# Kernel tuning notes

Measured on AMD Instinct MI355X. Metric: run time of the kernel, lower is better.

## Reference

```python
import jax, jax.numpy as jnp
import numpy as np

B, N, D, S = 16, 128, 128, 128   # batch, n_nodes, node/edge feat dim, state_dim
MP_INT = 256
UP_INT = 256
EPS = 1e-3  # keras BatchNormalization default epsilon


def _mlp(x, W1, b1, W2, b2):
    # Dense(relu) -> Dense(relu)
    h = jax.nn.relu(x @ W1 + b1)
    return jax.nn.relu(h @ W2 + b2)


def setup_inputs() -> dict:
    key = jax.random.key(0)
    ks = jax.random.split(key, 16)
    g = lambda k, shape: jax.random.normal(k, shape, dtype=jnp.float32) * 0.05
    nodes = jax.random.normal(ks[0], (B, N, D), dtype=jnp.float32)
    edges = jax.random.normal(ks[1], (B, N * N, D), dtype=jnp.float32)
    mask = (jax.random.uniform(ks[2], (B, N * N, 1)) > 0.5).astype(jnp.float32)
    return {
        "nodes": nodes, "edges": edges, "mask": mask,
        # Adj_Updater_1: concat(node_i, node_j, edge_ij) -> UP_INT -> S
        "W1a": g(ks[3], (3 * D, UP_INT)), "b1a": jnp.zeros((UP_INT,), jnp.float32),
        "W2a": g(ks[4], (UP_INT, S)), "b2a": jnp.zeros((S,), jnp.float32),
        # Message_Passer_1: concat(node_i, node_j, new_edge) -> MP_INT -> S
        "W1m": g(ks[5], (2 * D + S, MP_INT)), "b1m": jnp.zeros((MP_INT,), jnp.float32),
        "W2m": g(ks[6], (MP_INT, S)), "b2m": jnp.zeros((S,), jnp.float32),
        # Update_Func_1: concat(old_state, agg_messages) -> UP_INT -> S
        "W1u": g(ks[7], (D + S, UP_INT)), "b1u": jnp.zeros((UP_INT,), jnp.float32),
        "W2u": g(ks[8], (UP_INT, S)), "b2u": jnp.zeros((S,), jnp.float32),
        # BatchNorm (inference mode: moving stats) for nodes and edges
        "gamma_n": jnp.ones((S,), jnp.float32), "beta_n": jnp.zeros((S,), jnp.float32),
        "mean_n": jnp.zeros((S,), jnp.float32), "var_n": jnp.ones((S,), jnp.float32),
        "gamma_e": jnp.ones((S,), jnp.float32), "beta_e": jnp.zeros((S,), jnp.float32),
        "mean_e": jnp.zeros((S,), jnp.float32), "var_e": jnp.ones((S,), jnp.float32),
    }


def reference(nodes, edges, mask,
              W1a, b1a, W2a, b2a,
              W1m, b1m, W2m, b2m,
              W1u, b1u, W2u, b2u,
              gamma_n, beta_n, mean_n, var_n,
              gamma_e, beta_e, mean_e, var_e):
    b, n, d = nodes.shape
    # tf.tile(nodes,[1,n,1]): row p*n+q -> nodes[q]  (state_i)
    state_i = jnp.broadcast_to(nodes[:, None, :, :], (b, n, n, d)).reshape(b, n * n, d)
    # reshape(tile(nodes,[1,1,n])): row p*n+q -> nodes[p]  (state_j)
    state_j = jnp.broadcast_to(nodes[:, :, None, :], (b, n, n, d)).reshape(b, n * n, d)

    new_edges = _mlp(jnp.concatenate([state_i, state_j, edges], axis=-1), W1a, b1a, W2a, b2a)
    new_edges = new_edges * mask

    messages = _mlp(jnp.concatenate([state_i, state_j, new_edges], axis=-1), W1m, b1m, W2m, b2m)
    masked = (messages * mask).reshape(b, n, n, -1)
    agg_m = masked.sum(axis=2)  # reduce over axis 2 as in Message_Agg

    state_1 = _mlp(jnp.concatenate([nodes, agg_m], axis=-1), W1u, b1u, W2u, b2u)

    bn = lambda x, g_, b_, m_, v_: g_ * (x - m_) * jax.lax.rsqrt(v_ + EPS) + b_
    nodes_out = bn(state_1, gamma_n, beta_n, mean_n, var_n)
    edges_out = bn(new_edges, gamma_e, beta_e, mean_e, var_e)
    return nodes_out, edges_out
```

## Files before the change

### kernel.cpp

```cpp
#include <hip/hip_runtime.h>
#include <hip/hip_bf16.h>
#include <cstdint>
#include <cstddef>


typedef __attribute__((ext_vector_type(8))) __bf16 bf16x8;
typedef __attribute__((ext_vector_type(4))) float f32x4;

#define GLDS(gp, lp)                                                        \
  __builtin_amdgcn_global_load_lds(                                         \
      (const __attribute__((address_space(1))) void*)(gp),                  \
      (__attribute__((address_space(3))) void*)(lp), 16, 0, 0)

__device__ inline bf16x8 load8_cvt(const float* __restrict__ p) {
  const float4 a = *(const float4*)p;
  const float4 b = *(const float4*)(p + 4);
  bf16x8 r;
  r[0] = (__bf16)a.x; r[1] = (__bf16)a.y; r[2] = (__bf16)a.z; r[3] = (__bf16)a.w;
  r[4] = (__bf16)b.x; r[5] = (__bf16)b.y; r[6] = (__bf16)b.z; r[7] = (__bf16)b.w;
  return r;
}

__global__ void __launch_bounds__(256) proj_kernel(
    const float* __restrict__ nodes, const float* __restrict__ W1a,
    const float* __restrict__ b1a, const float* __restrict__ W1m,
    const float* __restrict__ b1m, const float* __restrict__ ge,
    const float* __restrict__ be, const float* __restrict__ me,
    const float* __restrict__ ve, float* __restrict__ outP) {
  __shared__ float x[8][128];
  const int mat = blockIdx.y;
  const int t = threadIdx.x;
  const float* W = (mat < 2 ? W1a : W1m) + ((mat & 1) ? 128 * 256 : 0);
  float* out = outP + (size_t)mat * (2048 * 256);
  const int r0 = blockIdx.x * 8;
  for (int i = t; i < 1024; i += 256)
    x[i >> 7][i & 127] = nodes[r0 * 128 + i];
  __syncthreads();
  float bv = 0.f;
  if (mat == 1) bv = b1a[t];
  if (mat == 3) {
    bv = b1m[t];
    const float* We = W1m + 65536;
    float cc = 0.f;
    for (int k = 0; k < 128; ++k) {
      float sc = ge[k] * rsqrtf(ve[k] + 1e-3f);
      float sh = be[k] - me[k] * sc;
      cc -= (sh / sc) * We[k * 256 + t];
    }
    bv += cc;
  }
  float acc[8];
#pragma unroll
  for (int r = 0; r < 8; ++r) acc[r] = bv;
  for (int k = 0; k < 128; ++k) {
    float w = W[k * 256 + t];
#pragma unroll
    for (int r = 0; r < 8; ++r) acc[r] += x[r][k] * w;
  }
  for (int r = 0; r < 8; ++r) out[(size_t)(r0 + r) * 256 + t] = acc[r];
}

__global__ void __launch_bounds__(256) wswz_kernel(
    const float* __restrict__ W1a, const float* __restrict__ W2a,
    const float* __restrict__ W1m, const float* __restrict__ W2m,
    const float* __restrict__ ge, const float* __restrict__ ve,
    __hip_bfloat16* __restrict__ dstp) {
  __bf16* dst = (__bf16*)dstp;
  const int mat = blockIdx.y;
  const float* src;
  __bf16* d;
  int nsh;
  if (mat == 0)      { src = W1a + 65536; d = dst;         nsh = 8; }
  else if (mat == 1) { src = W2a;         d = dst + 32768; nsh = 7; }
  else if (mat == 2) { src = W1m + 65536; d = dst + 65536; nsh = 8; }
  else               { src = W2m;         d = dst + 98304; nsh = 7; }
  const int nmask = (1 << nsh) - 1;
  const int base = (blockIdx.x * 256 + threadIdx.x) * 4;
#pragma unroll
  for (int i = 0; i < 4; ++i) {
    int s = base + i;
    int k = s >> nsh, n = s & nmask;
    float v = src[s];
    if (mat == 2) v *= sqrtf(ve[k] + 1e-3f) / ge[k];
    int g = k >> 3;
    if (nsh == 8) {
      int gs = (g & 8) | ((g ^ n) & 7);
      d[n * 128 + gs * 8 + (k & 7)] = (__bf16)v;
    } else {
      int gs = (g ^ n) & 7;
      d[((k >> 6) << 13) + (n << 6) + (gs << 3) + (k & 7)] = (__bf16)v;
    }
  }
}

__global__ void __launch_bounds__(256, 2) edge_mlp_kernel(
    const float* __restrict__ edges, const float* __restrict__ mask,
    const float* __restrict__ b2a, const float* __restrict__ ge,
    const float* __restrict__ be, const float* __restrict__ me,
    const float* __restrict__ ve, const float* __restrict__ Pa,
    const float* __restrict__ Qab, const __hip_bfloat16* __restrict__ Wsw,
    float* __restrict__ edges_out) {
  __shared__ __align__(16) char sW1h[16384];
  __shared__ __align__(16) char sW2h[16384];
  __shared__ __align__(16) char sH1q[16384];
  __shared__ float sQ[256];
  __shared__ float sB2[128];
  __shared__ float sMask[128];
  __shared__ float sScE[128];
  __shared__ float sShE[128];

  const int t = threadIdx.x;
  const int lane = t & 63, wv = t >> 6;
  const int cl = lane & 15, qd = lane >> 4;
  const int m0 = wv * 32;

  if (t < 128) {
    sB2[t] = b2a[t];
    float sc = ge[t] * rsqrtf(ve[t] + 1e-3f);
    sScE[t] = sc;
    sShE[t] = be[t] - me[t] * sc;
  }

  const int bb = blockIdx.x >> 5;
  const int p0 = (blockIdx.x & 31) * 4;
  const char* gW1base = (const char*)Wsw;
  const char* gW2base = (const char*)(Wsw + 32768);

  for (int tp = 0; tp < 4; ++tp) {
    const int p = p0 + tp;
    __syncthreads();
    sQ[t] = Qab[((bb << 7) + p) * 256 + t];
    if (t < 128) sMask[t] = mask[(bb << 14) + (p << 7) + t];

    const float* Xb = edges + ((size_t)((bb << 14) + (p << 7)) << 7);
    bf16x8 xf[2][4];
#pragma unroll
    for (int mt = 0; mt < 2; ++mt)
#pragma unroll
      for (int ks = 0; ks < 4; ++ks)
        xf[mt][ks] = load8_cvt(Xb + (m0 + mt * 16 + cl) * 128 + ks * 32 + qd * 8);

    f32x4 ne[2][8];
#pragma unroll
    for (int mt = 0; mt < 2; ++mt)
#pragma unroll
      for (int nt = 0; nt < 8; ++nt) {
        float bv = sB2[nt * 16 + cl];
        ne[mt][nt] = (f32x4){bv, bv, bv, bv};
      }

    for (int h = 0; h < 4; ++h) {
      __syncthreads();
      {
        const char* gW1 = gW1base + h * 16384;
        const char* gW2 = gW2base + h * 16384;
        for (int o = wv * 1024; o < 16384; o += 4096) {
          GLDS(gW1 + o + lane * 16, sW1h + o);
          GLDS(gW2 + o + lane * 16, sW2h + o);
        }
      }
      f32x4 a1[2][4];
#pragma unroll
      for (int mt = 0; mt < 2; ++mt)
#pragma unroll
        for (int nt = 0; nt < 4; ++nt) {
          const int col = h * 64 + nt * 16 + cl;
          const int mrow = m0 + mt * 16 + qd * 4;
          const float qv = sQ[col];
          const float* pa = Pa + (size_t)((bb << 7) + mrow) * 256 + col;
          a1[mt][nt] = (f32x4){pa[0] + qv, pa[256] + qv, pa[512] + qv, pa[768] + qv};
        }
      __syncthreads();
#pragma unroll
      for (int ks = 0; ks < 4; ++ks)
#pragma unroll
        for (int nt = 0; nt < 4; ++nt) {
          const int nl = nt * 16 + cl;
          const int g = ks * 4 + qd;
          const int gs = (g & 8) | ((g ^ nl) & 7);
          bf16x8 bw = *(const bf16x8*)(sW1h + nl * 256 + gs * 16);
          a1[0][nt] = __builtin_amdgcn_mfma_f32_16x16x32_bf16(xf[0][ks], bw, a1[0][nt], 0, 0, 0);
          a1[1][nt] = __builtin_amdgcn_mfma_f32_16x16x32_bf16(xf[1][ks], bw, a1[1][nt], 0, 0, 0);
        }
#pragma unroll
      for (int mt = 0; mt < 2; ++mt)
#pragma unroll
        for (int nt = 0; nt < 4; ++nt) {
          const int kq = nt * 16 + cl;
#pragma unroll
          for (int r = 0; r < 4; ++r) {
            const int m = m0 + mt * 16 + qd * 4 + r;
            float v = a1[mt][nt][r];
            v = v > 0.f ? v : 0.f;
            const int gs = ((kq >> 3) ^ m) & 7;
            *(__bf16*)(sH1q + m * 128 + gs * 16 + (kq & 7) * 2) = (__bf16)v;
          }
        }
      __syncthreads();
      bf16x8 hf[2][2];
#pragma unroll
      for (int mt = 0; mt < 2; ++mt)
#pragma unroll
        for (int ks = 0; ks < 2; ++ks) {
          const int m = m0 + mt * 16 + cl;
          const int g = ks * 4 + qd;
          const int gs = (g ^ m) & 7;
          hf[mt][ks] = *(const bf16x8*)(sH1q + m * 128 + gs * 16);
        }
#pragma unroll
      for (int ks = 0; ks < 2; ++ks)
#pragma unroll
        for (int nt = 0; nt < 8; ++nt) {
          const int n = nt * 16 + cl;
          const int g = ks * 4 + qd;
          const int gs = (g ^ n) & 7;
          bf16x8 bw = *(const bf16x8*)(sW2h + n * 128 + gs * 16);
          ne[0][nt] = __builtin_amdgcn_mfma_f32_16x16x32_bf16(hf[0][ks], bw, ne[0][nt], 0, 0, 0);
          ne[1][nt] = __builtin_amdgcn_mfma_f32_16x16x32_bf16(hf[1][ks], bw, ne[1][nt], 0, 0, 0);
        }
    }
    float* Ob = edges_out + ((size_t)((bb << 14) + (p << 7)) << 7);
#pragma unroll
    for (int mt = 0; mt < 2; ++mt)
#pragma unroll
      for (int nt = 0; nt < 8; ++nt) {
        const int col = nt * 16 + cl;
        const float sc = sScE[col], sh = sShE[col];
#pragma unroll
        for (int r = 0; r < 4; ++r) {
          const int m = m0 + mt * 16 + qd * 4 + r;
          float v = ne[mt][nt][r];
          v = v > 0.f ? v : 0.f;
          Ob[m * 128 + col] = (v * sMask[m]) * sc + sh;
        }
      }
  }
}

__global__ void __launch_bounds__(256, 2) msg_mlp_kernel(
    const float* __restrict__ mask, const float* __restrict__ b2m,
    const float* __restrict__ Pm, const float* __restrict__ Qmb,
    const __hip_bfloat16* __restrict__ Wsw, const float* __restrict__ Yedges,
    float* __restrict__ agg) {
  __shared__ __align__(16) char sW1h[16384];
  __shared__ __align__(16) char sW2h[16384];
  __shared__ __align__(16) char sH1q[16384];
  __shared__ float sQ[256];
  __shared__ float sB2[128];
  __shared__ float sMask[128];
  __shared__ float sAgg[512];

  const int t = threadIdx.x;
  const int lane = t & 63, wv = t >> 6;
  const int cl = lane & 15, qd = lane >> 4;
  const int m0 = wv * 32;

  if (t < 128) sB2[t] = b2m[t];

  const int bb = blockIdx.x >> 5;
  const int p0 = (blockIdx.x & 31) * 4;
  const char* gW1base = (const char*)Wsw;
  const char* gW2base = (const char*)(Wsw + 32768);

  for (int tp = 0; tp < 4; ++tp) {
    const int p = p0 + tp;
    __syncthreads();
    sQ[t] = Qmb[((bb << 7) + p) * 256 + t];
    if (t < 128) sMask[t] = mask[(bb << 14) + (p << 7) + t];

    const float* Xb = Yedges + ((size_t)((bb << 14) + (p << 7)) << 7);
    bf16x8 xf[2][4];
#pragma unroll
    for (int mt = 0; mt < 2; ++mt)
#pragma unroll
      for (int ks = 0; ks < 4; ++ks)
        xf[mt][ks] = load8_cvt(Xb + (m0 + mt * 16 + cl) * 128 + ks * 32 + qd * 8);

    f32x4 ms[2][8];
#pragma unroll
    for (int mt = 0; mt < 2; ++mt)
#pragma unroll
      for (int nt = 0; nt < 8; ++nt) {
        float bv = sB2[nt * 16 + cl];
        ms[mt][nt] = (f32x4){bv, bv, bv, bv};
      }

    for (int h = 0; h < 4; ++h) {
      __syncthreads();
      {
        const char* gW1 = gW1base + h * 16384;
        const char* gW2 = gW2base + h * 16384;
        for (int o = wv * 1024; o < 16384; o += 4096) {
          GLDS(gW1 + o + lane * 16, sW1h + o);
          GLDS(gW2 + o + lane * 16, sW2h + o);
        }
      }
      f32x4 a1[2][4];
#pragma unroll
      for (int mt = 0; mt < 2; ++mt)
#pragma unroll
        for (int nt = 0; nt < 4; ++nt) {
          const int col = h * 64 + nt * 16 + cl;
          const int mrow = m0 + mt * 16 + qd * 4;
          const float qv = sQ[col];
          const float* pa = Pm + (size_t)((bb << 7) + mrow) * 256 + col;
          a1[mt][nt] = (f32x4){pa[0] + qv, pa[256] + qv, pa[512] + qv, pa[768] + qv};
        }
      __syncthreads();
#pragma unroll
      for (int ks = 0; ks < 4; ++ks)
#pragma unroll
        for (int nt = 0; nt < 4; ++nt) {
          const int nl = nt * 16 + cl;
          const int g = ks * 4 + qd;
          const int gs = (g & 8) | ((g ^ nl) & 7);
          bf16x8 bw = *(const bf16x8*)(sW1h + nl * 256 + gs * 16);
          a1[0][nt] = __builtin_amdgcn_mfma_f32_16x16x32_bf16(xf[0][ks], bw, a1[0][nt], 0, 0, 0);
          a1[1][nt] = __builtin_amdgcn_mfma_f32_16x16x32_bf16(xf[1][ks], bw, a1[1][nt], 0, 0, 0);
        }
#pragma unroll
      for (int mt = 0; mt < 2; ++mt)
#pragma unroll
        for (int nt = 0; nt < 4; ++nt) {
          const int kq = nt * 16 + cl;
#pragma unroll
          for (int r = 0; r < 4; ++r) {
            const int m = m0 + mt * 16 + qd * 4 + r;
            float v = a1[mt][nt][r];
            v = v > 0.f ? v : 0.f;
            const int gs = ((kq >> 3) ^ m) & 7;
            *(__bf16*)(sH1q + m * 128 + gs * 16 + (kq & 7) * 2) = (__bf16)v;
          }
        }
      __syncthreads();
      bf16x8 hf[2][2];
#pragma unroll
      for (int mt = 0; mt < 2; ++mt)
#pragma unroll
        for (int ks = 0; ks < 2; ++ks) {
          const int m = m0 + mt * 16 + cl;
          const int g = ks * 4 + qd;
          const int gs = (g ^ m) & 7;
          hf[mt][ks] = *(const bf16x8*)(sH1q + m * 128 + gs * 16);
        }
#pragma unroll
      for (int ks = 0; ks < 2; ++ks)
#pragma unroll
        for (int nt = 0; nt < 8; ++nt) {
          const int n = nt * 16 + cl;
          const int g = ks * 4 + qd;
          const int gs = (g ^ n) & 7;
          bf16x8 bw = *(const bf16x8*)(sW2h + n * 128 + gs * 16);
          ms[0][nt] = __builtin_amdgcn_mfma_f32_16x16x32_bf16(hf[0][ks], bw, ms[0][nt], 0, 0, 0);
          ms[1][nt] = __builtin_amdgcn_mfma_f32_16x16x32_bf16(hf[1][ks], bw, ms[1][nt], 0, 0, 0);
        }
    }
#pragma unroll
    for (int nt = 0; nt < 8; ++nt) {
      float s = 0.f;
#pragma unroll
      for (int mt = 0; mt < 2; ++mt)
#pragma unroll
        for (int r = 0; r < 4; ++r) {
          const int m = m0 + mt * 16 + qd * 4 + r;
          float v = ms[mt][nt][r];
          v = v > 0.f ? v : 0.f;
          s += v * sMask[m];
        }
      s += __shfl_xor(s, 16);
      s += __shfl_xor(s, 32);
      if (lane < 16) sAgg[wv * 128 + nt * 16 + lane] = s;
    }
    __syncthreads();
    if (t < 128)
      agg[((bb << 7) + p) * 128 + t] =
          sAgg[t] + sAgg[128 + t] + sAgg[256 + t] + sAgg[384 + t];
  }
}

__global__ void __launch_bounds__(256) update_kernel(
    const float* __restrict__ nodes, const float* __restrict__ agg,
    const float* __restrict__ W1u, const float* __restrict__ b1u,
    const float* __restrict__ W2u, const float* __restrict__ b2u,
    const float* __restrict__ gn, const float* __restrict__ btn,
    const float* __restrict__ mn, const float* __restrict__ vn,
    float* __restrict__ out) {
  __shared__ float x[8][256];
  __shared__ float hh[8][256];
  const int t = threadIdx.x;
  const int r0 = blockIdx.x * 8;
  for (int i = t; i < 2048; i += 256) {
    int r = i >> 8, c = i & 255;
    x[r][c] = (c < 128) ? nodes[(r0 + r) * 128 + c] : agg[(r0 + r) * 128 + (c - 128)];
  }
  __syncthreads();
  float acc[8];
  {
    float bv = b1u[t];
#pragma unroll
    for (int r = 0; r < 8; ++r) acc[r] = bv;
  }
  for (int k = 0; k < 256; ++k) {
    float w = W1u[k * 256 + t];
#pragma unroll
    for (int r = 0; r < 8; ++r) acc[r] += x[r][k] * w;
  }
#pragma unroll
  for (int r = 0; r < 8; ++r) hh[r][t] = acc[r] > 0.f ? acc[r] : 0.f;
  __syncthreads();
  const int j = t & 127, half = t >> 7;
  float a2[4];
  {
    float bv = b2u[j];
#pragma unroll
    for (int r = 0; r < 4; ++r) a2[r] = bv;
  }
  for (int k = 0; k < 256; ++k) {
    float w = W2u[k * 128 + j];
#pragma unroll
    for (int r = 0; r < 4; ++r) a2[r] += hh[half * 4 + r][k] * w;
  }
  float sc = gn[j] * rsqrtf(vn[j] + 1e-3f);
  float sh = btn[j] - mn[j] * sc;
#pragma unroll
  for (int r = 0; r < 4; ++r) {
    float v = a2[r] > 0.f ? a2[r] : 0.f;
    out[(r0 + half * 4 + r) * 128 + j] = v * sc + sh;
  }
}

extern "C" void kernel_launch(void* const* d_in, const int* in_sizes, int n_in,
                              void* d_out, int out_size, void* d_ws,
                              size_t ws_size, hipStream_t stream) {
  (void)in_sizes; (void)n_in; (void)out_size; (void)ws_size;
  const float* nodes = (const float*)d_in[0];
  const float* edges = (const float*)d_in[1];
  const float* mask = (const float*)d_in[2];
  const float* W1a = (const float*)d_in[3];
  const float* b1a = (const float*)d_in[4];
  const float* W2a = (const float*)d_in[5];
  const float* b2a = (const float*)d_in[6];
  const float* W1m = (const float*)d_in[7];
  const float* b1m = (const float*)d_in[8];
  const float* W2m = (const float*)d_in[9];
  const float* b2m = (const float*)d_in[10];
  const float* W1u = (const float*)d_in[11];
  const float* b1u = (const float*)d_in[12];
  const float* W2u = (const float*)d_in[13];
  const float* b2u = (const float*)d_in[14];
  const float* gn = (const float*)d_in[15];
  const float* btn = (const float*)d_in[16];
  const float* mn = (const float*)d_in[17];
  const float* vn = (const float*)d_in[18];
  const float* ge = (const float*)d_in[19];
  const float* be = (const float*)d_in[20];
  const float* me = (const float*)d_in[21];
  const float* ve = (const float*)d_in[22];

  float* out_nodes = (float*)d_out;
  float* out_edges = (float*)d_out + 262144;

  char* ws = (char*)d_ws;
  float* Pa = (float*)(ws);
  float* Qab = (float*)(ws + ((size_t)1 << 21));
  float* Pm = (float*)(ws + ((size_t)2 << 21));
  float* Qmb = (float*)(ws + ((size_t)3 << 21));
  float* agg = (float*)(ws + ((size_t)4 << 21));
  __hip_bfloat16* Wsw = (__hip_bfloat16*)(ws + ((size_t)4 << 21) + ((size_t)1 << 20));

  proj_kernel<<<dim3(256, 4), 256, 0, stream>>>(nodes, W1a, b1a, W1m, b1m, ge,
                                                be, me, ve, Pa);
  wswz_kernel<<<dim3(32, 4), 256, 0, stream>>>(W1a, W2a, W1m, W2m, ge, ve, Wsw);
  edge_mlp_kernel<<<512, 256, 0, stream>>>(edges, mask, b2a, ge, be, me, ve, Pa,
                                           Qab, Wsw, out_edges);
  msg_mlp_kernel<<<512, 256, 0, stream>>>(mask, b2m, Pm, Qmb, Wsw + 65536,
                                          out_edges, agg);
  update_kernel<<<256, 256, 0, stream>>>(nodes, agg, W1u, b1u, W2u, b2u, gn, btn,
                                         mn, vn, out_nodes);
}
```

Before: 452.7 us.

## Fuse edge and message MLP kernels, passing new edges through LDS

Merges the edge-update MLP and the message MLP into one kernel, one block per (batch, row). The masked new-edge tile goes into shared memory as bf16 and feeds the message MLP directly, so the message pass no longer re-reads edges_out from global memory. The batchnorm folding into W1m and its bias is removed because the message MLP now consumes pre-BN values. Grid grows to 2048 blocks with 3 blocks per CU targeted, but each block now reloads the full weight set once instead of amortising it over four rows.

```diff
diff --git a/kernel.cpp b/kernel.cpp
--- a/kernel.cpp
+++ b/kernel.cpp
@@ -24,9 +24,7 @@
 __global__ void __launch_bounds__(256) proj_kernel(
     const float* __restrict__ nodes, const float* __restrict__ W1a,
     const float* __restrict__ b1a, const float* __restrict__ W1m,
-    const float* __restrict__ b1m, const float* __restrict__ ge,
-    const float* __restrict__ be, const float* __restrict__ me,
-    const float* __restrict__ ve, float* __restrict__ outP) {
+    const float* __restrict__ b1m, float* __restrict__ outP) {
   __shared__ float x[8][128];
   const int mat = blockIdx.y;
   const int t = threadIdx.x;
@@ -38,17 +36,7 @@
   __syncthreads();
   float bv = 0.f;
   if (mat == 1) bv = b1a[t];
-  if (mat == 3) {
-    bv = b1m[t];
-    const float* We = W1m + 65536;
-    float cc = 0.f;
-    for (int k = 0; k < 128; ++k) {
-      float sc = ge[k] * rsqrtf(ve[k] + 1e-3f);
-      float sh = be[k] - me[k] * sc;
-      cc -= (sh / sc) * We[k * 256 + t];
-    }
-    bv += cc;
-  }
+  if (mat == 3) bv = b1m[t];
   float acc[8];
 #pragma unroll
   for (int r = 0; r < 8; ++r) acc[r] = bv;
@@ -63,7 +51,6 @@
 __global__ void __launch_bounds__(256) wswz_kernel(
     const float* __restrict__ W1a, const float* __restrict__ W2a,
     const float* __restrict__ W1m, const float* __restrict__ W2m,
-    const float* __restrict__ ge, const float* __restrict__ ve,
     __hip_bfloat16* __restrict__ dstp) {
   __bf16* dst = (__bf16*)dstp;
   const int mat = blockIdx.y;
@@ -81,7 +68,6 @@
     int s = base + i;
     int k = s >> nsh, n = s & nmask;
     float v = src[s];
-    if (mat == 2) v *= sqrtf(ve[k] + 1e-3f) / ge[k];
     int g = k >> 3;
     if (nsh == 8) {
       int gs = (g & 8) | ((g ^ n) & 7);
@@ -93,289 +79,277 @@
   }
 }
 
-__global__ void __launch_bounds__(256, 2) edge_mlp_kernel(
+__global__ void __launch_bounds__(256, 3) fused_mlp_kernel(
     const float* __restrict__ edges, const float* __restrict__ mask,
-    const float* __restrict__ b2a, const float* __restrict__ ge,
-    const float* __restrict__ be, const float* __restrict__ me,
-    const float* __restrict__ ve, const float* __restrict__ Pa,
-    const float* __restrict__ Qab, const __hip_bfloat16* __restrict__ Wsw,
-    float* __restrict__ edges_out) {
-  __shared__ __align__(16) char sW1h[16384];
-  __shared__ __align__(16) char sW2h[16384];
-  __shared__ __align__(16) char sH1q[16384];
-  __shared__ float sQ[256];
-  __shared__ float sB2[128];
-  __shared__ float sMask[128];
-  __shared__ float sScE[128];
-  __shared__ float sShE[128];
+    const float* __restrict__ b2a, const float* __restrict__ b2m,
+    const float* __restrict__ ge, const float* __restrict__ be,
+    const float* __restrict__ me, const float* __restrict__ ve,
+    const float* __restrict__ Pa, const float* __restrict__ Qab,
+    const float* __restrict__ Pm, const float* __restrict__ Qmb,
+    const __hip_bfloat16* __restrict__ Wsw, float* __restrict__ edges_out,
+    float* __restrict__ agg) {
+  __shared__ __align__(16) char smem[53760];
+  char* sW1h = smem;
+  char* sW2h = smem + 16384;
+  char* sNE  = smem;
+  char* sH1q = smem + 32768;
+  float* sAgg = (float*)(smem + 32768);
+  float* sQa   = (float*)(smem + 49152);
+  float* sQm   = (float*)(smem + 50176);
+  float* sB2a  = (float*)(smem + 51200);
+  float* sB2m  = (float*)(smem + 51712);
+  float* sMask = (float*)(smem + 52224);
+  float* sScE  = (float*)(smem + 52736);
+  float* sShE  = (float*)(smem + 53248);
 
   const int t = threadIdx.x;
   const int lane = t & 63, wv = t >> 6;
   const int cl = lane & 15, qd = lane >> 4;
   const int m0 = wv * 32;
 
+  const int bb = blockIdx.x >> 7;
+  const int p = blockIdx.x & 127;
+
   if (t < 128) {
-    sB2[t] = b2a[t];
+    sB2a[t] = b2a[t];
+    sB2m[t] = b2m[t];
     float sc = ge[t] * rsqrtf(ve[t] + 1e-3f);
     sScE[t] = sc;
     sShE[t] = be[t] - me[t] * sc;
-  }
-
-  const int bb = blockIdx.x >> 5;
-  const int p0 = (blockIdx.x & 31) * 4;
-  const char* gW1base = (const char*)Wsw;
-  const char* gW2base = (const char*)(Wsw + 32768);
-
-  for (int tp = 0; tp < 4; ++tp) {
-    const int p = p0 + tp;
+    sMask[t] = mask[(bb << 14) + (p << 7) + t];
+  }
+  sQa[t] = Qab[((bb << 7) + p) * 256 + t];
+  sQm[t] = Qmb[((bb << 7) + p) * 256 + t];
+
+  const float* Xb = edges + ((size_t)((bb << 14) + (p << 7)) << 7);
+  bf16x8 xf[2][4];
+#pragma unroll
+  for (int mt = 0; mt < 2; ++mt)
+#pragma unroll
+    for (int ks = 0; ks < 4; ++ks)
+      xf[mt][ks] = load8_cvt(Xb + (m0 + mt * 16 + cl) * 128 + ks * 32 + qd * 8);
+
+  const char* gW1a_ = (const char*)Wsw;
+  const char* gW2a_ = (const char*)(Wsw + 32768);
+  const char* gW1m_ = (const char*)(Wsw + 65536);
+  const char* gW2m_ = (const char*)(Wsw + 98304);
+
+  __syncthreads();
+
+  f32x4 ne[2][8];
+#pragma unroll
+  for (int mt = 0; mt < 2; ++mt)
+#pragma unroll
+    for (int nt = 0; nt < 8; ++nt) {
+      float bv = sB2a[nt * 16 + cl];
+      ne[mt][nt] = (f32x4){bv, bv, bv, bv};
+    }
+
+  for (int h = 0; h < 4; ++h) {
+    if (h) __syncthreads();
+    {
+      const char* gW1 = gW1a_ + h * 16384;
+      const char* gW2 = gW2a_ + h * 16384;
+      for (int o = wv * 1024; o < 16384; o += 4096) {
+        GLDS(gW1 + o + lane * 16, sW1h + o);
+        GLDS(gW2 + o + lane * 16, sW2h + o);
+      }
+    }
+    f32x4 a1[2][4];
+#pragma unroll
+    for (int mt = 0; mt < 2; ++mt)
+#pragma unroll
+      for (int nt = 0; nt < 4; ++nt) {
+        const int col = h * 64 + nt * 16 + cl;
+        const int mrow = m0 + mt * 16 + qd * 4;
+        const float qv = sQa[col];
+        const float* pa = Pa + (size_t)((bb << 7) + mrow) * 256 + col;
+        a1[mt][nt] = (f32x4){pa[0] + qv, pa[256] + qv, pa[512] + qv, pa[768] + qv};
+      }
     __syncthreads();
-    sQ[t] = Qab[((bb << 7) + p) * 256 + t];
-    if (t < 128) sMask[t] = mask[(bb << 14) + (p << 7) + t];
-
-    const float* Xb = edges + ((size_t)((bb << 14) + (p << 7)) << 7);
-    bf16x8 xf[2][4];
-#pragma unroll
-    for (int mt = 0; mt < 2; ++mt)
-#pragma unroll
-      for (int ks = 0; ks < 4; ++ks)
-        xf[mt][ks] = load8_cvt(Xb + (m0 + mt * 16 + cl) * 128 + ks * 32 + qd * 8);
-
-    f32x4 ne[2][8];
-#pragma unroll
-    for (int mt = 0; mt < 2; ++mt)
-#pragma unroll
-      for (int nt = 0; nt < 8; ++nt) {
-        float bv = sB2[nt * 16 + cl];
-        ne[mt][nt] = (f32x4){bv, bv, bv, bv};
-      }
-
-    for (int h = 0; h < 4; ++h) {
-      __syncthreads();
-      {
-        const char* gW1 = gW1base + h * 16384;
-        const char* gW2 = gW2base + h * 16384;
-        for (int o = wv * 1024; o < 16384; o += 4096) {
-          GLDS(gW1 + o + lane * 16, sW1h + o);
-          GLDS(gW2 + o + lane * 16, sW2h + o);
-        }
-      }
-      f32x4 a1[2][4];
-#pragma unroll
-      for (int mt = 0; mt < 2; ++mt)
-#pragma unroll
-        for (int nt = 0; nt < 4; ++nt) {
-          const int col = h * 64 + nt * 16 + cl;
-          const int mrow = m0 + mt * 16 + qd * 4;
-          const float qv = sQ[col];
-          const float* pa = Pa + (size_t)((bb << 7) + mrow) * 256 + col;
-          a1[mt][nt] = (f32x4){pa[0] + qv, pa[256] + qv, pa[512] + qv, pa[768] + qv};
-        }
-      __syncthreads();
-#pragma unroll
-      for (int ks = 0; ks < 4; ++ks)
-#pragma unroll
-        for (int nt = 0; nt < 4; ++nt) {
-          const int nl = nt * 16 + cl;
-          const int g = ks * 4 + qd;
-          const int gs = (g & 8) | ((g ^ nl) & 7);
-          bf16x8 bw = *(const bf16x8*)(sW1h + nl * 256 + gs * 16);
-          a1[0][nt] = __builtin_amdgcn_mfma_f32_16x16x32_bf16(xf[0][ks], bw, a1[0][nt], 0, 0, 0);
-          a1[1][nt] = __builtin_amdgcn_mfma_f32_16x16x32_bf16(xf[1][ks], bw, a1[1][nt], 0, 0, 0);
-        }
-#pragma unroll
-      for (int mt = 0; mt < 2; ++mt)
-#pragma unroll
-        for (int nt = 0; nt < 4; ++nt) {
-          const int kq = nt * 16 + cl;
-#pragma unroll
-          for (int r = 0; r < 4; ++r) {
-            const int m = m0 + mt * 16 + qd * 4 + r;
-            float v = a1[mt][nt][r];
-            v = v > 0.f ? v : 0.f;
-            const int gs = ((kq >> 3) ^ m) & 7;
-            *(__bf16*)(sH1q + m * 128 + gs * 16 + (kq & 7) * 2) = (__bf16)v;
-          }
-        }
-      __syncthreads();
-      bf16x8 hf[2][2];
-#pragma unroll
-      for (int mt = 0; mt < 2; ++mt)
-#pragma unroll
-        for (int ks = 0; ks < 2; ++ks) {
-          const int m = m0 + mt * 16 + cl;
-          const int g = ks * 4 + qd;
-          const int gs = (g ^ m) & 7;
-          hf[mt][ks] = *(const bf16x8*)(sH1q + m * 128 + gs * 16);
-        }
-#pragma unroll
-      for (int ks = 0; ks < 2; ++ks)
-#pragma unroll
-        for (int nt = 0; nt < 8; ++nt) {
-          const int n = nt * 16 + cl;
-          const int g = ks * 4 + qd;
-          const int gs = (g ^ n) & 7;
-          bf16x8 bw = *(const bf16x8*)(sW2h + n * 128 + gs * 16);
-          ne[0][nt] = __builtin_amdgcn_mfma_f32_16x16x32_bf16(hf[0][ks], bw, ne[0][nt], 0, 0, 0);
-          ne[1][nt] = __builtin_amdgcn_mfma_f32_16x16x32_bf16(hf[1][ks], bw, ne[1][nt], 0, 0, 0);
-        }
-    }
-    float* Ob = edges_out + ((size_t)((bb << 14) + (p << 7)) << 7);
-#pragma unroll
-    for (int mt = 0; mt < 2; ++mt)
-#pragma unroll
-      for (int nt = 0; nt < 8; ++nt) {
-        const int col = nt * 16 + cl;
-        const float sc = sScE[col], sh = sShE[col];
+#pragma unroll
+    for (int ks = 0; ks < 4; ++ks)
+#pragma unroll
+      for (int nt = 0; nt < 4; ++nt) {
+        const int nl = nt * 16 + cl;
+        const int g = ks * 4 + qd;
+        const int gs = (g & 8) | ((g ^ nl) & 7);
+        bf16x8 bw = *(const bf16x8*)(sW1h + nl * 256 + gs * 16);
+        a1[0][nt] = __builtin_amdgcn_mfma_f32_16x16x32_bf16(xf[0][ks], bw, a1[0][nt], 0, 0, 0);
+        a1[1][nt] = __builtin_amdgcn_mfma_f32_16x16x32_bf16(xf[1][ks], bw, a1[1][nt], 0, 0, 0);
+      }
+#pragma unroll
+    for (int mt = 0; mt < 2; ++mt)
+#pragma unroll
+      for (int nt = 0; nt < 4; ++nt) {
+        const int kq = nt * 16 + cl;
 #pragma unroll
         for (int r = 0; r < 4; ++r) {
           const int m = m0 + mt * 16 + qd * 4 + r;
-          float v = ne[mt][nt][r];
+          float v = a1[mt][nt][r];
           v = v > 0.f ? v : 0.f;
-          Ob[m * 128 + col] = (v * sMask[m]) * sc + sh;
+          const int gs = ((kq >> 3) ^ m) & 7;
+          *(__bf16*)(sH1q + m * 128 + gs * 16 + (kq & 7) * 2) = (__bf16)v;
         }
       }
-  }
-}
-
-__global__ void __launch_bounds__(256, 2) msg_mlp_kernel(
-    const float* __restrict__ mask, const float* __restrict__ b2m,
-    const float* __restrict__ Pm, const float* __restrict__ Qmb,
-    const __hip_bfloat16* __restrict__ Wsw, const float* __restrict__ Yedges,
-    float* __restrict__ agg) {
-  __shared__ __align__(16) char sW1h[16384];
-  __shared__ __align__(16) char sW2h[16384];
-  __shared__ __align__(16) char sH1q[16384];
-  __shared__ float sQ[256];
-  __shared__ float sB2[128];
-  __shared__ float sMask[128];
-  __shared__ float sAgg[512];
-
-  const int t = threadIdx.x;
-  const int lane = t & 63, wv = t >> 6;
-  const int cl = lane & 15, qd = lane >> 4;
-  const int m0 = wv * 32;
-
-  if (t < 128) sB2[t] = b2m[t];
-
-  const int bb = blockIdx.x >> 5;
-  const int p0 = (blockIdx.x & 31) * 4;
-  const char* gW1base = (const char*)Wsw;
-  const char* gW2base = (const char*)(Wsw + 32768);
-
-  for (int tp = 0; tp < 4; ++tp) {
-    const int p = p0 + tp;
     __syncthreads();
-    sQ[t] = Qmb[((bb << 7) + p) * 256 + t];
-    if (t < 128) sMask[t] = mask[(bb << 14) + (p << 7) + t];
-
-    const float* Xb = Yedges + ((size_t)((bb << 14) + (p << 7)) << 7);
-    bf16x8 xf[2][4];
-#pragma unroll
-    for (int mt = 0; mt < 2; ++mt)
-#pragma unroll
-      for (int ks = 0; ks < 4; ++ks)
-        xf[mt][ks] = load8_cvt(Xb + (m0 + mt * 16 + cl) * 128 + ks * 32 + qd * 8);
-
-    f32x4 ms[2][8];
-#pragma unroll
-    for (int mt = 0; mt < 2; ++mt)
+    bf16x8 hf[2][2];
+#pragma unroll
+    for (int mt = 0; mt < 2; ++mt)
+#pragma unroll
+      for (int ks = 0; ks < 2; ++ks) {
+        const int m = m0 + mt * 16 + cl;
+        const int g = ks * 4 + qd;
+        const int gs = (g ^ m) & 7;
+        hf[mt][ks] = *(const bf16x8*)(sH1q + m * 128 + gs * 16);
+      }
+#pragma unroll
+    for (int ks = 0; ks < 2; ++ks)
 #pragma unroll
       for (int nt = 0; nt < 8; ++nt) {
-        float bv = sB2[nt * 16 + cl];
-        ms[mt][nt] = (f32x4){bv, bv, bv, bv};
-      }
-
-    for (int h = 0; h < 4; ++h) {
-      __syncthreads();
-      {
-        const char* gW1 = gW1base + h * 16384;
-        const char* gW2 = gW2base + h * 16384;
-        for (int o = wv * 1024; o < 16384; o += 4096) {
-          GLDS(gW1 + o + lane * 16, sW1h + o);
-          GLDS(gW2 + o + lane * 16, sW2h + o);
-        }
-      }
-      f32x4 a1[2][4];
-#pragma unroll
-      for (int mt = 0; mt < 2; ++mt)
-#pragma unroll
-        for (int nt = 0; nt < 4; ++nt) {
-          const int col = h * 64 + nt * 16 + cl;
-          const int mrow = m0 + mt * 16 + qd * 4;
-          const float qv = sQ[col];
-          const float* pa = Pm + (size_t)((bb << 7) + mrow) * 256 + col;
-          a1[mt][nt] = (f32x4){pa[0] + qv, pa[256] + qv, pa[512] + qv, pa[768] + qv};
-        }
-      __syncthreads();
-#pragma unroll
-      for (int ks = 0; ks < 4; ++ks)
-#pragma unroll
-        for (int nt = 0; nt < 4; ++nt) {
-          const int nl = nt * 16 + cl;
-          const int g = ks * 4 + qd;
-          const int gs = (g & 8) | ((g ^ nl) & 7);
-          bf16x8 bw = *(const bf16x8*)(sW1h + nl * 256 + gs * 16);
-          a1[0][nt] = __builtin_amdgcn_mfma_f32_16x16x32_bf16(xf[0][ks], bw, a1[0][nt], 0, 0, 0);
-          a1[1][nt] = __builtin_amdgcn_mfma_f32_16x16x32_bf16(xf[1][ks], bw, a1[1][nt], 0, 0, 0);
-        }
-#pragma unroll
-      for (int mt = 0; mt < 2; ++mt)
-#pragma unroll
-        for (int nt = 0; nt < 4; ++nt) {
-          const int kq = nt * 16 + cl;
-#pragma unroll
-          for (int r = 0; r < 4; ++r) {
-            const int m = m0 + mt * 16 + qd * 4 + r;
-            float v = a1[mt][nt][r];
-            v = v > 0.f ? v : 0.f;
-            const int gs = ((kq >> 3) ^ m) & 7;
-            *(__bf16*)(sH1q + m * 128 + gs * 16 + (kq & 7) * 2) = (__bf16)v;
-          }
-        }
-      __syncthreads();
-      bf16x8 hf[2][2];
-#pragma unroll
-      for (int mt = 0; mt < 2; ++mt)
-#pragma unroll
-        for (int ks = 0; ks < 2; ++ks) {
-          const int m = m0 + mt * 16 + cl;
-          const int g = ks * 4 + qd;
-          const int gs = (g ^ m) & 7;
-          hf[mt][ks] = *(const bf16x8*)(sH1q + m * 128 + gs * 16);
-        }
-#pragma unroll
-      for (int ks = 0; ks < 2; ++ks)
-#pragma unroll
-        for (int nt = 0; nt < 8; ++nt) {
-          const int n = nt * 16 + cl;
-          const int g = ks * 4 + qd;
-          const int gs = (g ^ n) & 7;
-          bf16x8 bw = *(const bf16x8*)(sW2h + n * 128 + gs * 16);
-          ms[0][nt] = __builtin_amdgcn_mfma_f32_16x16x32_bf16(hf[0][ks], bw, ms[0][nt], 0, 0, 0);
-          ms[1][nt] = __builtin_amdgcn_mfma_f32_16x16x32_bf16(hf[1][ks], bw, ms[1][nt], 0, 0, 0);
-        }
-    }
+        const int n = nt * 16 + cl;
+        const int g = ks * 4 + qd;
+        const int gs = (g ^ n) & 7;
+        bf16x8 bw = *(const bf16x8*)(sW2h + n * 128 + gs * 16);
+        ne[0][nt] = __builtin_amdgcn_mfma_f32_16x16x32_bf16(hf[0][ks], bw, ne[0][nt], 0, 0, 0);
+        ne[1][nt] = __builtin_amdgcn_mfma_f32_16x16x32_bf16(hf[1][ks], bw, ne[1][nt], 0, 0, 0);
+      }
+  }
+
+  __syncthreads();
+  float* Ob = edges_out + ((size_t)((bb << 14) + (p << 7)) << 7);
+#pragma unroll
+  for (int mt = 0; mt < 2; ++mt)
 #pragma unroll
     for (int nt = 0; nt < 8; ++nt) {
-      float s = 0.f;
-#pragma unroll
-      for (int mt = 0; mt < 2; ++mt)
+      const int col = nt * 16 + cl;
+      const float scv = sScE[col], shv = sShE[col];
+      const int g = col >> 3;
+#pragma unroll
+      for (int r = 0; r < 4; ++r) {
+        const int m = m0 + mt * 16 + qd * 4 + r;
+        float v = ne[mt][nt][r];
+        v = v > 0.f ? v : 0.f;
+        v *= sMask[m];
+        const int gs = (g & 8) | ((g ^ m) & 7);
+        *(__bf16*)(sNE + m * 256 + gs * 16 + (col & 7) * 2) = (__bf16)v;
+        Ob[m * 128 + col] = v * scv + shv;
+      }
+    }
+  __syncthreads();
+  bf16x8 xfm[2][4];
+#pragma unroll
+  for (int mt = 0; mt < 2; ++mt)
+#pragma unroll
+    for (int ks = 0; ks < 4; ++ks) {
+      const int m = m0 + mt * 16 + cl;
+      const int g = ks * 4 + qd;
+      const int gs = (g & 8) | ((g ^ m) & 7);
+      xfm[mt][ks] = *(const bf16x8*)(sNE + m * 256 + gs * 16);
+    }
+  __syncthreads();
+
+  f32x4 ms[2][8];
+#pragma unroll
+  for (int mt = 0; mt < 2; ++mt)
+#pragma unroll
+    for (int nt = 0; nt < 8; ++nt) {
+      float bv = sB2m[nt * 16 + cl];
+      ms[mt][nt] = (f32x4){bv, bv, bv, bv};
+    }
+
+  for (int h = 0; h < 4; ++h) {
+    if (h) __syncthreads();
+    {
+      const char* gW1 = gW1m_ + h * 16384;
+      const char* gW2 = gW2m_ + h * 16384;
+      for (int o = wv * 1024; o < 16384; o += 4096) {
+        GLDS(gW1 + o + lane * 16, sW1h + o);
+        GLDS(gW2 + o + lane * 16, sW2h + o);
+      }
+    }
+    f32x4 a1[2][4];
+#pragma unroll
+    for (int mt = 0; mt < 2; ++mt)
+#pragma unroll
+      for (int nt = 0; nt < 4; ++nt) {
+        const int col = h * 64 + nt * 16 + cl;
+        const int mrow = m0 + mt * 16 + qd * 4;
+        const float qv = sQm[col];
+        const float* pa = Pm + (size_t)((bb << 7) + mrow) * 256 + col;
+        a1[mt][nt] = (f32x4){pa[0] + qv, pa[256] + qv, pa[512] + qv, pa[768] + qv};
+      }
+    __syncthreads();
+#pragma unroll
+    for (int ks = 0; ks < 4; ++ks)
+#pragma unroll
+      for (int nt = 0; nt < 4; ++nt) {
+        const int nl = nt * 16 + cl;
+        const int g = ks * 4 + qd;
+        const int gs = (g & 8) | ((g ^ nl) & 7);
+        bf16x8 bw = *(const bf16x8*)(sW1h + nl * 256 + gs * 16);
+        a1[0][nt] = __builtin_amdgcn_mfma_f32_16x16x32_bf16(xfm[0][ks], bw, a1[0][nt], 0, 0, 0);
+        a1[1][nt] = __builtin_amdgcn_mfma_f32_16x16x32_bf16(xfm[1][ks], bw, a1[1][nt], 0, 0, 0);
+      }
+#pragma unroll
+    for (int mt = 0; mt < 2; ++mt)
+#pragma unroll
+      for (int nt = 0; nt < 4; ++nt) {
+        const int kq = nt * 16 + cl;
 #pragma unroll
         for (int r = 0; r < 4; ++r) {
           const int m = m0 + mt * 16 + qd * 4 + r;
-          float v = ms[mt][nt][r];
+          float v = a1[mt][nt][r];
           v = v > 0.f ? v : 0.f;
-          s += v * sMask[m];
+          const int gs = ((kq >> 3) ^ m) & 7;
+          *(__bf16*)(sH1q + m * 128 + gs * 16 + (kq & 7) * 2) = (__bf16)v;
         }
-      s += __shfl_xor(s, 16);
-      s += __shfl_xor(s, 32);
-      if (lane < 16) sAgg[wv * 128 + nt * 16 + lane] = s;
-    }
+      }
     __syncthreads();
-    if (t < 128)
-      agg[((bb << 7) + p) * 128 + t] =
-          sAgg[t] + sAgg[128 + t] + sAgg[256 + t] + sAgg[384 + t];
-  }
+    bf16x8 hf[2][2];
+#pragma unroll
+    for (int mt = 0; mt < 2; ++mt)
+#pragma unroll
+      for (int ks = 0; ks < 2; ++ks) {
+        const int m = m0 + mt * 16 + cl;
+        const int g = ks * 4 + qd;
+        const int gs = (g ^ m) & 7;
+        hf[mt][ks] = *(const bf16x8*)(sH1q + m * 128 + gs * 16);
+      }
+#pragma unroll
+    for (int ks = 0; ks < 2; ++ks)
+#pragma unroll
+      for (int nt = 0; nt < 8; ++nt) {
+        const int n = nt * 16 + cl;
+        const int g = ks * 4 + qd;
+        const int gs = (g ^ n) & 7;
+        bf16x8 bw = *(const bf16x8*)(sW2h + n * 128 + gs * 16);
+        ms[0][nt] = __builtin_amdgcn_mfma_f32_16x16x32_bf16(hf[0][ks], bw, ms[0][nt], 0, 0, 0);
+        ms[1][nt] = __builtin_amdgcn_mfma_f32_16x16x32_bf16(hf[1][ks], bw, ms[1][nt], 0, 0, 0);
+      }
+  }
+
+  __syncthreads();
+#pragma unroll
+  for (int nt = 0; nt < 8; ++nt) {
+    float s = 0.f;
+#pragma unroll
+    for (int mt = 0; mt < 2; ++mt)
+#pragma unroll
+      for (int r = 0; r < 4; ++r) {
+        const int m = m0 + mt * 16 + qd * 4 + r;
+        float v = ms[mt][nt][r];
+        v = v > 0.f ? v : 0.f;
+        s += v * sMask[m];
+      }
+    s += __shfl_xor(s, 16);
+    s += __shfl_xor(s, 32);
+    if (lane < 16) sAgg[wv * 128 + nt * 16 + lane] = s;
+  }
+  __syncthreads();
+  if (t < 128)
+    agg[((bb << 7) + p) * 128 + t] =
+        sAgg[t] + sAgg[128 + t] + sAgg[256 + t] + sAgg[384 + t];
 }
 
 __global__ void __launch_bounds__(256) update_kernel(
@@ -468,13 +442,11 @@
   float* agg = (float*)(ws + ((size_t)4 << 21));
   __hip_bfloat16* Wsw = (__hip_bfloat16*)(ws + ((size_t)4 << 21) + ((size_t)1 << 20));
 
-  proj_kernel<<<dim3(256, 4), 256, 0, stream>>>(nodes, W1a, b1a, W1m, b1m, ge,
-                                                be, me, ve, Pa);
-  wswz_kernel<<<dim3(32, 4), 256, 0, stream>>>(W1a, W2a, W1m, W2m, ge, ve, Wsw);
-  edge_mlp_kernel<<<512, 256, 0, stream>>>(edges, mask, b2a, ge, be, me, ve, Pa,
-                                           Qab, Wsw, out_edges);
-  msg_mlp_kernel<<<512, 256, 0, stream>>>(mask, b2m, Pm, Qmb, Wsw + 65536,
-                                          out_edges, agg);
+  proj_kernel<<<dim3(256, 4), 256, 0, stream>>>(nodes, W1a, b1a, W1m, b1m, Pa);
+  wswz_kernel<<<dim3(32, 4), 256, 0, stream>>>(W1a, W2a, W1m, W2m, Wsw);
+  fused_mlp_kernel<<<2048, 256, 0, stream>>>(edges, mask, b2a, b2m, ge, be, me,
+                                             ve, Pa, Qab, Pm, Qmb, Wsw,
+                                             out_edges, agg);
   update_kernel<<<256, 256, 0, stream>>>(nodes, agg, W1u, b1u, W2u, b2u, gn, btn,
                                          mn, vn, out_nodes);
 }
```

Result: slower. 550.6 us (+21.6%).
